# Kernel optimization log

Measured on AMD Instinct MI355X. Metric: run time of the kernel, lower is better.

Reference implementation:

```python
import jax, jax.numpy as jnp
import numpy as np

B, L = 4, 2048
D_MODEL = 64          # d_model = input_size
ED = 128              # d_inner = expand_factor * d_model = hidden_size
N = 32                # d_state
DCONV = 16            # d_conv
NLAYERS = 4
DTRANK = 4            # ceil(d_model/16)
NCLS = 1
EPS = 1e-5


def setup_inputs() -> dict:
    key = jax.random.key(0)
    ks = jax.random.split(key, 10)
    g = lambda k, s, sc: jax.random.normal(k, s, dtype=jnp.float32) * sc
    inp = {}
    inp["x"] = jax.random.normal(ks[0], (B, L, D_MODEL), dtype=jnp.float32)
    inp["in_w"] = g(ks[1], (NLAYERS, 2 * ED, D_MODEL), 0.1)
    inp["in_b"] = jnp.zeros((NLAYERS, 2 * ED), jnp.float32)
    inp["conv_w"] = g(ks[2], (NLAYERS, ED, 1, DCONV), 0.1)  # depthwise kernel (OIH per group)
    inp["conv_b"] = jnp.zeros((NLAYERS, ED), jnp.float32)
    inp["xproj_w"] = g(ks[3], (NLAYERS, DTRANK + 2 * N, ED), 0.1)
    inp["dtproj_w"] = g(ks[4], (NLAYERS, ED, DTRANK), 0.5)
    inp["dtproj_b"] = g(ks[5], (NLAYERS, ED), 0.5)
    # S4D-real init: A[e, n] = n+1
    A = jnp.tile(jnp.arange(1, N + 1, dtype=jnp.float32), (ED, 1))
    inp["A_log"] = jnp.tile(jnp.log(A)[None], (NLAYERS, 1, 1))
    inp["Dp"] = jnp.ones((NLAYERS, ED), jnp.float32)
    inp["outproj_w"] = g(ks[6], (NLAYERS, D_MODEL, ED), 0.1)
    inp["outproj_b"] = jnp.zeros((NLAYERS, D_MODEL), jnp.float32)
    inp["norm_w"] = jnp.ones((NLAYERS, D_MODEL), jnp.float32)
    inp["fc_w"] = g(ks[7], (NCLS, ED), 0.1)
    inp["fc_b"] = jnp.zeros((NCLS,), jnp.float32)
    return inp


def _rmsnorm(x, w):
    return x * jax.lax.rsqrt(jnp.mean(x * x, axis=-1, keepdims=True) + EPS) * w


def _causal_dwconv(x, w, b):
    # x: [B,L,ED], w: [ED,1,DCONV] depthwise, causal left pad
    xt = jnp.swapaxes(x, 1, 2)  # [B,ED,L]
    y = jax.lax.conv_general_dilated(
        xt, w, window_strides=(1,), padding=[(DCONV - 1, 0)],
        dimension_numbers=("NCH", "OIH", "NCH"), feature_group_count=ED)
    return jnp.swapaxes(y, 1, 2) + b


def _mamba_block(h, in_w, in_b, conv_w, conv_b, xproj_w, dtproj_w, dtproj_b,
                 A_log, Dp, outproj_w, outproj_b, last):
    xz = jnp.einsum("bld,ed->ble", h, in_w) + in_b          # [B,L,2ED]
    xin, z = jnp.split(xz, 2, axis=-1)
    xc = jax.nn.silu(_causal_dwconv(xin, conv_w, conv_b))    # [B,L,ED]
    dbc = jnp.einsum("ble,re->blr", xc, xproj_w)             # [B,L,DTRANK+2N]
    delta = dbc[..., :DTRANK]
    Bm = dbc[..., DTRANK:DTRANK + N]                          # [B,L,N]
    Cm = dbc[..., DTRANK + N:]                                # [B,L,N]
    delta = jax.nn.softplus(jnp.einsum("blr,er->ble", delta, dtproj_w) + dtproj_b)
    A = -jnp.exp(A_log)                                       # [ED,N]
    dA = jnp.exp(delta[..., None] * A)                        # [B,L,ED,N]
    dBu = delta[..., None] * Bm[:, :, None, :] * xc[..., None]  # [B,L,ED,N]

    def step(hs, t):
        dA_t, dBu_t, C_t = t                                  # [B,ED,N],[B,ED,N],[B,N]
        hs = dA_t * hs + dBu_t
        y = jnp.einsum("ben,bn->be", hs, C_t)
        return hs, y

    h0 = jnp.zeros((xc.shape[0], ED, N), dtype=xc.dtype)
    _, ys = jax.lax.scan(step, h0, (jnp.swapaxes(dA, 0, 1),
                                    jnp.swapaxes(dBu, 0, 1),
                                    jnp.swapaxes(Cm, 0, 1)))
    y = jnp.swapaxes(ys, 0, 1) + Dp * xc                      # [B,L,ED]
    y = y * jax.nn.silu(z)
    if last:
        return y                                              # classifier taps d_inner features
    return jnp.einsum("ble,de->bld", y, outproj_w) + outproj_b


def reference(x, in_w, in_b, conv_w, conv_b, xproj_w, dtproj_w, dtproj_b,
              A_log, Dp, outproj_w, outproj_b, norm_w, fc_w, fc_b):
    h = x
    for i in range(NLAYERS - 1):
        h = h + _mamba_block(_rmsnorm(h, norm_w[i]), in_w[i], in_b[i], conv_w[i],
                             conv_b[i], xproj_w[i], dtproj_w[i], dtproj_b[i],
                             A_log[i], Dp[i], outproj_w[i], outproj_b[i], False)
    i = NLAYERS - 1
    y = _mamba_block(_rmsnorm(h, norm_w[i]), in_w[i], in_b[i], conv_w[i],
                     conv_b[i], xproj_w[i], dtproj_w[i], dtproj_b[i],
                     A_log[i], Dp[i], outproj_w[i], outproj_b[i], True)
    last_hidden = y[:, -1, :]                                 # [B,ED]
    return last_hidden @ fc_w.T + fc_b                        # [B,NCLS]
```

## Files before the change

### kernel.cpp

```cpp
#include <hip/hip_runtime.h>
#include <math.h>

#define BSZ 4
#define Lseq 2048
#define DM 64
#define ED 128
#define NST 32
#define DCONVK 16
#define NLAYERS 4
#define DTRANK 4
#define EPSV 1e-5f
#define NC 128
#define LC (Lseq / NC)
#define TT 16

__device__ __forceinline__ float sigf(float x) { return 1.0f / (1.0f + __expf(-x)); }
__device__ __forceinline__ float hsum4(float4 a) { return (a.x + a.y) + (a.z + a.w); }

__global__ __launch_bounds__(256) void k_layer_gemm(
    const float* __restrict__ hin, const float* __restrict__ norm_w,
    const float* __restrict__ in_w, const float* __restrict__ in_b,
    float* __restrict__ xin, float* __restrict__ zb)
{
    const int t0 = blockIdx.x * TT;
    const int tid = threadIdx.x;
    const int lane = tid & 63;
    const int wv = tid >> 6;
    __shared__ __align__(16) float hn[TT][DM];

    const float nw = norm_w[lane];
    float hval[4];
    #pragma unroll
    for (int j = 0; j < 4; ++j)
        hval[j] = hin[(size_t)(t0 + wv * 4 + j) * DM + lane];

    #pragma unroll
    for (int j = 0; j < 4; ++j) {
        float ss = hval[j] * hval[j];
        #pragma unroll
        for (int off = 32; off; off >>= 1) ss += __shfl_xor(ss, off, 64);
        const float sc = rsqrtf(ss * (1.0f / DM) + EPSV);
        hn[wv * 4 + j][lane] = hval[j] * sc * nw;
    }
    __syncthreads();

    {
        float4 w4[16];
        const float4* wr = (const float4*)(in_w + tid * DM);
        #pragma unroll
        for (int i = 0; i < 16; ++i) w4[i] = wr[i];
        const float bias = in_b[tid];
        #pragma unroll 2
        for (int tok = 0; tok < TT; ++tok) {
            const float4* hv4 = (const float4*)&hn[tok][0];
            float4 a4 = make_float4(0.f, 0.f, 0.f, 0.f);
            #pragma unroll
            for (int i = 0; i < 16; ++i) {
                float4 hv = hv4[i];
                a4.x = fmaf(hv.x, w4[i].x, a4.x);
                a4.y = fmaf(hv.y, w4[i].y, a4.y);
                a4.z = fmaf(hv.z, w4[i].z, a4.z);
                a4.w = fmaf(hv.w, w4[i].w, a4.w);
            }
            const float r = bias + hsum4(a4);
            if (tid < ED) xin[(size_t)(t0 + tok) * ED + tid] = r;
            else          zb[(size_t)(t0 + tok) * ED + (tid - ED)] = r;
        }
    }
}

__global__ __launch_bounds__(256) void k_conv_scan(
    const float* __restrict__ xin, const float* __restrict__ conv_w,
    const float* __restrict__ conv_b, const float* __restrict__ xproj_w,
    const float* __restrict__ dtproj_w, const float* __restrict__ dtproj_b,
    const float* __restrict__ A_log,
    float* __restrict__ xc_out, float* __restrict__ delta_out,
    float* __restrict__ Bout, float* __restrict__ Cout,
    float* __restrict__ aprod, float* __restrict__ hloc)
{
    const int blk = blockIdx.x;
    const int b   = blk >> 7;
    const int c   = blk & 127;
    const int l0  = c * TT;
    const size_t t0 = (size_t)b * Lseq + l0;
    const int tid = threadIdx.x;
    __shared__ __align__(16) float xs[(TT + DCONVK - 1) * ED];
    __shared__ __align__(16) float xcs[TT][ED];
    __shared__ __align__(16) float Bs[TT][NST];
    __shared__ float dts[TT][DTRANK];
    float (*dl)[ED] = (float (*)[ED])xs;

    {
        const int NV = (TT + DCONVK - 1) * ED / 4;
        for (int idx4 = tid; idx4 < NV; idx4 += 256) {
            const int row = idx4 >> 5;
            const int lrow = l0 - (DCONVK - 1) + row;
            float4 v = make_float4(0.f, 0.f, 0.f, 0.f);
            if (lrow >= 0)
                v = ((const float4*)(xin + ((size_t)b * Lseq + lrow) * ED))[idx4 & 31];
            ((float4*)xs)[idx4] = v;
        }
    }
    __syncthreads();

    const int e = tid & 127, half = tid >> 7;
    {
        float w[DCONVK];
        {
            const float4* cw = (const float4*)(conv_w + e * DCONVK);
            #pragma unroll
            for (int i = 0; i < 4; ++i) {
                float4 cc = cw[i];
                w[i*4+0] = cc.x; w[i*4+1] = cc.y; w[i*4+2] = cc.z; w[i*4+3] = cc.w;
            }
        }
        const float cb = conv_b[e];
        #pragma unroll 2
        for (int j = 0; j < 8; ++j) {
            const int tok = half * 8 + j;
            float acc = cb;
            #pragma unroll
            for (int k = 0; k < DCONVK; ++k)
                acc = fmaf(xs[(tok + k) * ED + e], w[k], acc);
            const float xcv = acc * sigf(acc);
            xcs[tok][e] = xcv;
            xc_out[(t0 + tok) * ED + e] = xcv;
        }
    }
    __syncthreads();

    {
        const int wv = tid >> 6, lane = tid & 63;
        float4 acc[4];
        #pragma unroll
        for (int j = 0; j < 4; ++j) acc[j] = make_float4(0.f, 0.f, 0.f, 0.f);
        #pragma unroll 1
        for (int p = 0; p < 4; ++p) {
            float4 w4[8];
            const float4* wr = (const float4*)(xproj_w + lane * ED + p * 32);
            #pragma unroll
            for (int i = 0; i < 8; ++i) w4[i] = wr[i];
            #pragma unroll
            for (int j = 0; j < 4; ++j) {
                const float4* yv = (const float4*)&xcs[wv * 4 + j][p * 32];
                #pragma unroll
                for (int i = 0; i < 8; ++i) {
                    float4 hv = yv[i];
                    acc[j].x = fmaf(hv.x, w4[i].x, acc[j].x);
                    acc[j].y = fmaf(hv.y, w4[i].y, acc[j].y);
                    acc[j].z = fmaf(hv.z, w4[i].z, acc[j].z);
                    acc[j].w = fmaf(hv.w, w4[i].w, acc[j].w);
                }
            }
        }
        #pragma unroll
        for (int j = 0; j < 4; ++j) {
            const int tok = wv * 4 + j;
            const float v = hsum4(acc[j]);
            if (lane < DTRANK) {
                dts[tok][lane] = v;
            } else if (lane < DTRANK + NST) {
                Bs[tok][lane - DTRANK] = v;
                Bout[(t0 + tok) * NST + (lane - DTRANK)] = v;
            } else {
                Cout[(t0 + tok) * NST + (lane - DTRANK - NST)] = v;
            }
        }
        {
            const int ridx = lane & 3;
            const int ks   = (lane >> 2) & 3;
            const int tsub = lane >> 4;
            const int r4   = 64 + ridx;
            const int tok  = wv * 4 + tsub;
            const float4* wr = (const float4*)(xproj_w + r4 * ED + ks * 32);
            const float4* yv = (const float4*)&xcs[tok][ks * 32];
            float4 a4 = make_float4(0.f, 0.f, 0.f, 0.f);
            #pragma unroll
            for (int i = 0; i < 8; ++i) {
                float4 hv = yv[i]; float4 wv4 = wr[i];
                a4.x = fmaf(hv.x, wv4.x, a4.x);
                a4.y = fmaf(hv.y, wv4.y, a4.y);
                a4.z = fmaf(hv.z, wv4.z, a4.z);
                a4.w = fmaf(hv.w, wv4.w, a4.w);
            }
            float v = hsum4(a4);
            v += __shfl_xor(v, 4, 64);
            v += __shfl_xor(v, 8, 64);
            if (ks == 0) Cout[(t0 + tok) * NST + (r4 - DTRANK - NST)] = v;
        }
    }
    __syncthreads();

    {
        const float4 dwv = *(const float4*)(dtproj_w + e * DTRANK);
        const float bias = dtproj_b[e];
        #pragma unroll 2
        for (int j = 0; j < 8; ++j) {
            const int tok = half * 8 + j;
            float a = bias;
            a = fmaf(dts[tok][0], dwv.x, a);
            a = fmaf(dts[tok][1], dwv.y, a);
            a = fmaf(dts[tok][2], dwv.z, a);
            a = fmaf(dts[tok][3], dwv.w, a);
            const float sp = fmaxf(a, 0.f) + log1pf(__expf(-fabsf(a)));
            dl[tok][e] = sp;
            delta_out[(t0 + tok) * ED + e] = sp;
        }
    }
    __syncthreads();

    {
        float dsum = 0.f;
        #pragma unroll 4
        for (int l = 0; l < TT; ++l) dsum += dl[l][e];

        #pragma unroll 1
        for (int g = 0; g < 2; ++g) {
            const int n0 = half * 16 + g * 8;
            float Aen[8];
            {
                const float4* a4 = (const float4*)(A_log + e * NST + n0);
                const float4 v0 = a4[0], v1 = a4[1];
                Aen[0] = -__expf(v0.x); Aen[1] = -__expf(v0.y);
                Aen[2] = -__expf(v0.z); Aen[3] = -__expf(v0.w);
                Aen[4] = -__expf(v1.x); Aen[5] = -__expf(v1.y);
                Aen[6] = -__expf(v1.z); Aen[7] = -__expf(v1.w);
            }
            float hs[8];
            #pragma unroll
            for (int k = 0; k < 8; ++k) hs[k] = 0.f;
            #pragma unroll 2
            for (int l = 0; l < TT; ++l) {
                const float de   = dl[l][e];
                const float dexc = de * xcs[l][e];
                const float4 B0 = *(const float4*)&Bs[l][n0];
                const float4 B1 = *(const float4*)&Bs[l][n0 + 4];
                float a;
                a = __expf(de * Aen[0]); hs[0] = fmaf(a, hs[0], B0.x * dexc);
                a = __expf(de * Aen[1]); hs[1] = fmaf(a, hs[1], B0.y * dexc);
                a = __expf(de * Aen[2]); hs[2] = fmaf(a, hs[2], B0.z * dexc);
                a = __expf(de * Aen[3]); hs[3] = fmaf(a, hs[3], B0.w * dexc);
                a = __expf(de * Aen[4]); hs[4] = fmaf(a, hs[4], B1.x * dexc);
                a = __expf(de * Aen[5]); hs[5] = fmaf(a, hs[5], B1.y * dexc);
                a = __expf(de * Aen[6]); hs[6] = fmaf(a, hs[6], B1.z * dexc);
                a = __expf(de * Aen[7]); hs[7] = fmaf(a, hs[7], B1.w * dexc);
            }
            const size_t idx = (((size_t)b * NC + c) * ED + e) * NST + n0;
            *(float4*)(hloc + idx)     = make_float4(hs[0], hs[1], hs[2], hs[3]);
            *(float4*)(hloc + idx + 4) = make_float4(hs[4], hs[5], hs[6], hs[7]);
            *(float4*)(aprod + idx) =
                make_float4(__expf(Aen[0] * dsum), __expf(Aen[1] * dsum),
                            __expf(Aen[2] * dsum), __expf(Aen[3] * dsum));
            *(float4*)(aprod + idx + 4) =
                make_float4(__expf(Aen[4] * dsum), __expf(Aen[5] * dsum),
                            __expf(Aen[6] * dsum), __expf(Aen[7] * dsum));
        }
    }
}

__global__ __launch_bounds__(256) void k_scan_combine(
    const float* __restrict__ aprod, float* __restrict__ hloc,
    float* __restrict__ hend)
{
    const int tid = blockIdx.x * 256 + threadIdx.x;
    const int b = tid >> 12;
    const int en = tid & 4095;
    size_t idx = (size_t)b * NC * (ED * NST) + en;
    float h = 0.f;
    #pragma unroll 4
    for (int c = 0; c < NC; ++c) {
        const float a = aprod[idx];
        const float u = hloc[idx];
        hloc[idx] = h;
        h = fmaf(a, h, u);
        idx += ED * NST;
    }
    hend[(size_t)b * (ED * NST) + en] = h;
}

__global__ __launch_bounds__(256) void k_scan_gemm(
    const float* __restrict__ delta, const float* __restrict__ Bv,
    const float* __restrict__ Cv, const float* __restrict__ xc,
    const float* __restrict__ zbin, const float* __restrict__ A_log,
    const float* __restrict__ Dp, const float* __restrict__ hinit,
    const float* __restrict__ ow, const float* __restrict__ ob,
    const float* __restrict__ hin, const float* __restrict__ norm_w,
    const float* __restrict__ in_w, const float* __restrict__ in_b,
    float* __restrict__ hout, float* __restrict__ xin, float* __restrict__ zb)
{
    const int blk = blockIdx.x;
    const int b   = blk >> 7;
    const int c   = blk & 127;
    const int l0  = c * TT;
    const size_t t0 = (size_t)b * Lseq + l0;
    const int tid = threadIdx.x;
    const int e = tid & 127, half = tid >> 7;

    __shared__ __align__(16) float dlS[TT][ED];
    __shared__ __align__(16) float xcS[TT][ED];
    __shared__ __align__(16) float BsS[TT][NST];
    __shared__ __align__(16) float CsS[TT][NST];
    __shared__ __align__(16) float ys[TT][ED];
    __shared__ __align__(16) float pp[2][TT][ED];
    __shared__ __align__(16) float hn[TT][DM];

    {
        const float4* dsrc = (const float4*)(delta + t0 * ED);
        const float4* xsrc = (const float4*)(xc + t0 * ED);
        float4* ddst = (float4*)&dlS[0][0];
        float4* xdst = (float4*)&xcS[0][0];
        #pragma unroll
        for (int i = 0; i < 2; ++i) {
            ddst[tid + i * 256] = dsrc[tid + i * 256];
            xdst[tid + i * 256] = xsrc[tid + i * 256];
        }
        if (tid < 128) {
            ((float4*)&BsS[0][0])[tid] = ((const float4*)(Bv + t0 * NST))[tid];
            ((float4*)&CsS[0][0])[tid] = ((const float4*)(Cv + t0 * NST))[tid];
        }
    }
    __syncthreads();

    #pragma unroll 1
    for (int g = 0; g < 2; ++g) {
        const int n0 = half * 16 + g * 8;
        float Aen[8];
        {
            const float4* a4 = (const float4*)(A_log + e * NST + n0);
            const float4 v0 = a4[0], v1 = a4[1];
            Aen[0] = -__expf(v0.x); Aen[1] = -__expf(v0.y);
            Aen[2] = -__expf(v0.z); Aen[3] = -__expf(v0.w);
            Aen[4] = -__expf(v1.x); Aen[5] = -__expf(v1.y);
            Aen[6] = -__expf(v1.z); Aen[7] = -__expf(v1.w);
        }
        float hs[8];
        {
            const size_t idx = (((size_t)b * NC + c) * ED + e) * NST + n0;
            const float4 h0 = *(const float4*)(hinit + idx);
            const float4 h1 = *(const float4*)(hinit + idx + 4);
            hs[0] = h0.x; hs[1] = h0.y; hs[2] = h0.z; hs[3] = h0.w;
            hs[4] = h1.x; hs[5] = h1.y; hs[6] = h1.z; hs[7] = h1.w;
        }
        #pragma unroll 2
        for (int l = 0; l < TT; ++l) {
            const float de   = dlS[l][e];
            const float dexc = de * xcS[l][e];
            const float4 B0 = *(const float4*)&BsS[l][n0];
            const float4 B1 = *(const float4*)&BsS[l][n0 + 4];
            const float4 C0 = *(const float4*)&CsS[l][n0];
            const float4 C1 = *(const float4*)&CsS[l][n0 + 4];
            float a, p = 0.f;
            a = __expf(de * Aen[0]); hs[0] = fmaf(a, hs[0], B0.x * dexc); p = fmaf(hs[0], C0.x, p);
            a = __expf(de * Aen[1]); hs[1] = fmaf(a, hs[1], B0.y * dexc); p = fmaf(hs[1], C0.y, p);
            a = __expf(de * Aen[2]); hs[2] = fmaf(a, hs[2], B0.z * dexc); p = fmaf(hs[2], C0.z, p);
            a = __expf(de * Aen[3]); hs[3] = fmaf(a, hs[3], B0.w * dexc); p = fmaf(hs[3], C0.w, p);
            a = __expf(de * Aen[4]); hs[4] = fmaf(a, hs[4], B1.x * dexc); p = fmaf(hs[4], C1.x, p);
            a = __expf(de * Aen[5]); hs[5] = fmaf(a, hs[5], B1.y * dexc); p = fmaf(hs[5], C1.y, p);
            a = __expf(de * Aen[6]); hs[6] = fmaf(a, hs[6], B1.z * dexc); p = fmaf(hs[6], C1.z, p);
            a = __expf(de * Aen[7]); hs[7] = fmaf(a, hs[7], B1.w * dexc); p = fmaf(hs[7], C1.w, p);
            if (g == 0) pp[half][l][e] = p;
            else        pp[half][l][e] += p;
        }
    }
    __syncthreads();
    {
        const float dpe = Dp[e];
        #pragma unroll 2
        for (int j = 0; j < 8; ++j) {
            const int tl = half * 8 + j;
            const size_t tok = t0 + tl;
            const float p = pp[0][tl][e] + pp[1][tl][e];
            const float zi = zbin[tok * ED + e];
            ys[tl][e] = (p + dpe * xcS[tl][e]) * (zi * sigf(zi));
        }
    }
    __syncthreads();

    const int lane = tid & 63;
    const int wv = tid >> 6;
    const float nw = norm_w[lane];
    float hval[4];
    {
        float4 acc[4];
        #pragma unroll
        for (int j = 0; j < 4; ++j) acc[j] = make_float4(0.f, 0.f, 0.f, 0.f);
        #pragma unroll 1
        for (int p = 0; p < 4; ++p) {
            float4 w4[8];
            const float4* wr = (const float4*)(ow + lane * ED + p * 32);
            #pragma unroll
            for (int i = 0; i < 8; ++i) w4[i] = wr[i];
            #pragma unroll
            for (int j = 0; j < 4; ++j) {
                const float4* yv = (const float4*)&ys[wv * 4 + j][p * 32];
                #pragma unroll
                for (int i = 0; i < 8; ++i) {
                    float4 hv = yv[i];
                    acc[j].x = fmaf(hv.x, w4[i].x, acc[j].x);
                    acc[j].y = fmaf(hv.y, w4[i].y, acc[j].y);
                    acc[j].z = fmaf(hv.z, w4[i].z, acc[j].z);
                    acc[j].w = fmaf(hv.w, w4[i].w, acc[j].w);
                }
            }
        }
        const float obd = ob[lane];
        #pragma unroll
        for (int j = 0; j < 4; ++j) {
            const size_t tok = t0 + wv * 4 + j;
            hval[j] = hsum4(acc[j]) + obd + hin[tok * DM + lane];
            hout[tok * DM + lane] = hval[j];
        }
    }
    #pragma unroll
    for (int j = 0; j < 4; ++j) {
        float ss = hval[j] * hval[j];
        #pragma unroll
        for (int off = 32; off; off >>= 1) ss += __shfl_xor(ss, off, 64);
        const float sc = rsqrtf(ss * (1.0f / DM) + EPSV);
        hn[wv * 4 + j][lane] = hval[j] * sc * nw;
    }
    __syncthreads();
    {
        float4 w4[16];
        const float4* wr = (const float4*)(in_w + tid * DM);
        #pragma unroll
        for (int i = 0; i < 16; ++i) w4[i] = wr[i];
        const float bias = in_b[tid];
        #pragma unroll 2
        for (int tok = 0; tok < TT; ++tok) {
            const float4* hv4 = (const float4*)&hn[tok][0];
            float4 a4 = make_float4(0.f, 0.f, 0.f, 0.f);
            #pragma unroll
            for (int i = 0; i < 16; ++i) {
                float4 hv = hv4[i];
                a4.x = fmaf(hv.x, w4[i].x, a4.x);
                a4.y = fmaf(hv.y, w4[i].y, a4.y);
                a4.z = fmaf(hv.z, w4[i].z, a4.z);
                a4.w = fmaf(hv.w, w4[i].w, a4.w);
            }
            const float r = bias + hsum4(a4);
            if (tid < ED) xin[(size_t)(t0 + tok) * ED + tid] = r;
            else          zb[(size_t)(t0 + tok) * ED + (tid - ED)] = r;
        }
    }
}

__global__ __launch_bounds__(128) void k_final_last(
    const float* __restrict__ hend, const float* __restrict__ Cv,
    const float* __restrict__ xc, const float* __restrict__ zb,
    const float* __restrict__ Dp, const float* __restrict__ fcw,
    const float* __restrict__ fcb, float* __restrict__ out)
{
    const int b = blockIdx.x;
    const int e = threadIdx.x;
    const size_t tok = (size_t)b * Lseq + (Lseq - 1);
    const float* hp = hend + (size_t)b * (ED * NST) + e * NST;
    const float* cp = Cv + tok * NST;
    float p = 0.f;
    #pragma unroll
    for (int n = 0; n < NST; ++n) p = fmaf(hp[n], cp[n], p);
    const float xce = xc[tok * ED + e];
    const float zi  = zb[tok * ED + e];
    float val = (p + Dp[e] * xce) * (zi * sigf(zi)) * fcw[e];
    __shared__ float sred[2];
    #pragma unroll
    for (int off = 32; off; off >>= 1) val += __shfl_xor(val, off, 64);
    if ((threadIdx.x & 63) == 0) sred[threadIdx.x >> 6] = val;
    __syncthreads();
    if (threadIdx.x == 0) out[b] = sred[0] + sred[1] + fcb[0];
}

extern "C" void kernel_launch(void* const* d_in, const int* in_sizes, int n_in,
                              void* d_out, int out_size, void* d_ws, size_t ws_size,
                              hipStream_t stream)
{
    const float* x         = (const float*)d_in[0];
    const float* in_w      = (const float*)d_in[1];
    const float* in_b      = (const float*)d_in[2];
    const float* conv_w    = (const float*)d_in[3];
    const float* conv_b    = (const float*)d_in[4];
    const float* xproj_w   = (const float*)d_in[5];
    const float* dtproj_w  = (const float*)d_in[6];
    const float* dtproj_b  = (const float*)d_in[7];
    const float* A_log     = (const float*)d_in[8];
    const float* Dp        = (const float*)d_in[9];
    const float* outproj_w = (const float*)d_in[10];
    const float* outproj_b = (const float*)d_in[11];
    const float* norm_w    = (const float*)d_in[12];
    const float* fc_w      = (const float*)d_in[13];
    const float* fc_b      = (const float*)d_in[14];

    const size_t TOK = (size_t)BSZ * Lseq;
    float* ws = (float*)d_ws;
    float* h0    = ws; ws += TOK * DM;
    float* h1    = ws; ws += TOK * DM;
    float* xin   = ws; ws += TOK * ED;
    float* zbuf  = ws; ws += TOK * ED;
    float* xc    = ws; ws += TOK * ED;
    float* dlt   = ws; ws += TOK * ED;
    float* Bv    = ws; ws += TOK * NST;
    float* Cv    = ws; ws += TOK * NST;
    float* aprod = ws; ws += (size_t)BSZ * NC * ED * NST;
    float* hloc  = ws; ws += (size_t)BSZ * NC * ED * NST;
    float* hend  = ws; ws += (size_t)BSZ * ED * NST;

    const float* hres = x;
    float* hbufs[2] = { h0, h1 };

    k_layer_gemm<<<(int)(TOK / TT), 256, 0, stream>>>(
        x, norm_w, in_w, in_b, xin, zbuf);

    for (int i = 0; i < NLAYERS; ++i) {
        const int last = (i == NLAYERS - 1);
        const float* Alog_i = A_log + (size_t)i * ED * NST;
        k_conv_scan<<<(int)(BSZ * NC), 256, 0, stream>>>(
            xin, conv_w + (size_t)i * ED * DCONVK, conv_b + (size_t)i * ED,
            xproj_w + (size_t)i * (DTRANK + 2 * NST) * ED,
            dtproj_w + (size_t)i * ED * DTRANK, dtproj_b + (size_t)i * ED,
            Alog_i, xc, dlt, Bv, Cv, aprod, hloc);
        k_scan_combine<<<(BSZ * ED * NST) / 256, 256, 0, stream>>>(
            aprod, hloc, hend);
        if (!last) {
            float* hout = hbufs[i & 1];
            k_scan_gemm<<<(int)(BSZ * NC), 256, 0, stream>>>(
                dlt, Bv, Cv, xc, zbuf, Alog_i, Dp + (size_t)i * ED, hloc,
                outproj_w + (size_t)i * DM * ED, outproj_b + (size_t)i * DM,
                hres, norm_w + (size_t)(i + 1) * DM,
                in_w + (size_t)(i + 1) * 2 * ED * DM,
                in_b + (size_t)(i + 1) * 2 * ED,
                hout, xin, zbuf);
            hres = hout;
        } else {
            k_final_last<<<BSZ, 128, 0, stream>>>(
                hend, Cv, xc, zbuf, Dp + (size_t)i * ED, fc_w, fc_b, (float*)d_out);
        }
    }
}
```

Baseline: 382.9 us.

## Fuse all Mamba layers into one persistent cooperative kernel with grid syncs

Replaces the sequence of per-layer kernel launches with a single cooperative kernel of 512 blocks that loops over layers and separates phases with grid.sync(). Per-block intermediates (conv output, delta, B, C, residual) stay in shared memory and registers, so the global round-trips for xc, delta, B, C and the residual stream are no longer needed. It also removes about a dozen launch gaps. The cost is grid-wide barriers, and the chunk-combine phase runs on only 64 blocks while the rest wait. If the cooperative launch fails, the code falls back to the old multi-kernel path.

New measurement: 1.106 ms. 189% more time.

```diff
diff --git a/kernel.cpp b/kernel.cpp
--- a/kernel.cpp
+++ b/kernel.cpp
@@ -1,5 +1,8 @@
 #include <hip/hip_runtime.h>
+#include <hip/hip_cooperative_groups.h>
 #include <math.h>
+
+namespace cg = cooperative_groups;
 
 #define BSZ 4
 #define Lseq 2048
@@ -11,11 +14,392 @@
 #define DTRANK 4
 #define EPSV 1e-5f
 #define NC 128
-#define LC (Lseq / NC)
 #define TT 16
 
 __device__ __forceinline__ float sigf(float x) { return 1.0f / (1.0f + __expf(-x)); }
 __device__ __forceinline__ float hsum4(float4 a) { return (a.x + a.y) + (a.z + a.w); }
+
+struct Params {
+    const float *x, *in_w, *in_b, *conv_w, *conv_b, *xproj_w, *dtproj_w, *dtproj_b;
+    const float *A_log, *Dp, *outproj_w, *outproj_b, *norm_w, *fc_w, *fc_b;
+    float *out, *xin, *zbuf, *aprod, *hloc, *hend;
+};
+
+__device__ __forceinline__ void inproj16(
+    const float* in_w_l, const float* in_b_l, const float (*hn)[DM],
+    float* xin, float* zbuf, size_t t0, int tid)
+{
+    float4 w4[16];
+    const float4* wr = (const float4*)(in_w_l + tid * DM);
+    #pragma unroll
+    for (int i = 0; i < 16; ++i) w4[i] = wr[i];
+    const float bias = in_b_l[tid];
+    #pragma unroll 2
+    for (int tok = 0; tok < TT; ++tok) {
+        const float4* hv4 = (const float4*)&hn[tok][0];
+        float4 a4 = make_float4(0.f, 0.f, 0.f, 0.f);
+        #pragma unroll
+        for (int i = 0; i < 16; ++i) {
+            float4 hv = hv4[i];
+            a4.x = fmaf(hv.x, w4[i].x, a4.x);
+            a4.y = fmaf(hv.y, w4[i].y, a4.y);
+            a4.z = fmaf(hv.z, w4[i].z, a4.z);
+            a4.w = fmaf(hv.w, w4[i].w, a4.w);
+        }
+        const float r = bias + hsum4(a4);
+        if (tid < ED) xin[(t0 + tok) * ED + tid] = r;
+        else          zbuf[(t0 + tok) * ED + (tid - ED)] = r;
+    }
+}
+
+__global__ __launch_bounds__(256) void k_mamba_fused(Params P)
+{
+    cg::grid_group grid = cg::this_grid();
+    const int blk = blockIdx.x;
+    const int b   = blk >> 7;
+    const int c   = blk & 127;
+    const int l0  = c * TT;
+    const size_t t0 = (size_t)b * Lseq + l0;
+    const int tid = threadIdx.x;
+    const int e = tid & 127, half = tid >> 7;
+    const int lane = tid & 63, wv = tid >> 6;
+    const int e2 = tid >> 1, nh = tid & 1;
+
+    __shared__ __align__(16) float smem[7168];
+    float (*xcs)[ED] = (float (*)[ED])smem;
+    float (*Bs)[NST] = (float (*)[NST])(smem + 2048);
+    float (*Cs)[NST] = (float (*)[NST])(smem + 2560);
+    float* uni = smem + 3072;
+    float* xs = uni;
+    float (*dts)[DTRANK] = (float (*)[DTRANK])(uni + 3968);
+    float (*dl)[ED] = (float (*)[ED])uni;
+    float (*ys)[ED] = (float (*)[ED])(uni + 2048);
+    float (*hn)[DM] = (float (*)[DM])(smem + 2048);
+    float* sred = uni;
+
+    float hres[4];
+
+    {
+        const float nw = P.norm_w[lane];
+        #pragma unroll
+        for (int j = 0; j < 4; ++j)
+            hres[j] = P.x[(size_t)(t0 + wv * 4 + j) * DM + lane];
+        #pragma unroll
+        for (int j = 0; j < 4; ++j) {
+            float ss = hres[j] * hres[j];
+            #pragma unroll
+            for (int off = 32; off; off >>= 1) ss += __shfl_xor(ss, off, 64);
+            const float sc = rsqrtf(ss * (1.0f / DM) + EPSV);
+            hn[wv * 4 + j][lane] = hres[j] * sc * nw;
+        }
+        __syncthreads();
+        inproj16(P.in_w, P.in_b, hn, P.xin, P.zbuf, t0, tid);
+    }
+    grid.sync();
+
+    #pragma unroll 1
+    for (int i = 0; i < NLAYERS; ++i) {
+        const float* conv_w_i = P.conv_w + (size_t)i * ED * DCONVK;
+        const float* conv_b_i = P.conv_b + (size_t)i * ED;
+        const float* xproj_i  = P.xproj_w + (size_t)i * (DTRANK + 2 * NST) * ED;
+        const float* dtw_i    = P.dtproj_w + (size_t)i * ED * DTRANK;
+        const float* dtb_i    = P.dtproj_b + (size_t)i * ED;
+        const float* Alog_i   = P.A_log + (size_t)i * ED * NST;
+        const float* Dp_i     = P.Dp + (size_t)i * ED;
+
+        {
+            const int NV = (TT + DCONVK - 1) * ED / 4;
+            for (int idx4 = tid; idx4 < NV; idx4 += 256) {
+                const int row = idx4 >> 5;
+                const int lrow = l0 - (DCONVK - 1) + row;
+                float4 v = make_float4(0.f, 0.f, 0.f, 0.f);
+                if (lrow >= 0)
+                    v = ((const float4*)(P.xin + ((size_t)b * Lseq + lrow) * ED))[idx4 & 31];
+                ((float4*)xs)[idx4] = v;
+            }
+        }
+        __syncthreads();
+        {
+            float w[DCONVK];
+            {
+                const float4* cw = (const float4*)(conv_w_i + e * DCONVK);
+                #pragma unroll
+                for (int q = 0; q < 4; ++q) {
+                    float4 cc = cw[q];
+                    w[q*4+0] = cc.x; w[q*4+1] = cc.y; w[q*4+2] = cc.z; w[q*4+3] = cc.w;
+                }
+            }
+            const float cb = conv_b_i[e];
+            #pragma unroll 2
+            for (int j = 0; j < 8; ++j) {
+                const int tok = half * 8 + j;
+                float acc = cb;
+                #pragma unroll
+                for (int k = 0; k < DCONVK; ++k)
+                    acc = fmaf(xs[(tok + k) * ED + e], w[k], acc);
+                const float xcv = acc * sigf(acc);
+                xcs[tok][e] = xcv;
+            }
+        }
+        __syncthreads();
+        {
+            float4 acc[4];
+            #pragma unroll
+            for (int j = 0; j < 4; ++j) acc[j] = make_float4(0.f, 0.f, 0.f, 0.f);
+            #pragma unroll 1
+            for (int p = 0; p < 4; ++p) {
+                float4 w4[8];
+                const float4* wr = (const float4*)(xproj_i + lane * ED + p * 32);
+                #pragma unroll
+                for (int q = 0; q < 8; ++q) w4[q] = wr[q];
+                #pragma unroll
+                for (int j = 0; j < 4; ++j) {
+                    const float4* yv = (const float4*)&xcs[wv * 4 + j][p * 32];
+                    #pragma unroll
+                    for (int q = 0; q < 8; ++q) {
+                        float4 hv = yv[q];
+                        acc[j].x = fmaf(hv.x, w4[q].x, acc[j].x);
+                        acc[j].y = fmaf(hv.y, w4[q].y, acc[j].y);
+                        acc[j].z = fmaf(hv.z, w4[q].z, acc[j].z);
+                        acc[j].w = fmaf(hv.w, w4[q].w, acc[j].w);
+                    }
+                }
+            }
+            #pragma unroll
+            for (int j = 0; j < 4; ++j) {
+                const int tok = wv * 4 + j;
+                const float v = hsum4(acc[j]);
+                if (lane < DTRANK)            dts[tok][lane] = v;
+                else if (lane < DTRANK + NST) Bs[tok][lane - DTRANK] = v;
+                else                          Cs[tok][lane - DTRANK - NST] = v;
+            }
+            {
+                const int ridx = lane & 3;
+                const int ks   = (lane >> 2) & 3;
+                const int tsub = lane >> 4;
+                const int r4   = 64 + ridx;
+                const int tok  = wv * 4 + tsub;
+                const float4* wr = (const float4*)(xproj_i + r4 * ED + ks * 32);
+                const float4* yv = (const float4*)&xcs[tok][ks * 32];
+                float4 a4 = make_float4(0.f, 0.f, 0.f, 0.f);
+                #pragma unroll
+                for (int q = 0; q < 8; ++q) {
+                    float4 hv = yv[q]; float4 wv4 = wr[q];
+                    a4.x = fmaf(hv.x, wv4.x, a4.x);
+                    a4.y = fmaf(hv.y, wv4.y, a4.y);
+                    a4.z = fmaf(hv.z, wv4.z, a4.z);
+                    a4.w = fmaf(hv.w, wv4.w, a4.w);
+                }
+                float v = hsum4(a4);
+                v += __shfl_xor(v, 4, 64);
+                v += __shfl_xor(v, 8, 64);
+                if (ks == 0) Cs[tok][r4 - DTRANK - NST] = v;
+            }
+        }
+        __syncthreads();
+        {
+            const float4 dwv = *(const float4*)(dtw_i + e * DTRANK);
+            const float bias = dtb_i[e];
+            #pragma unroll 2
+            for (int j = 0; j < 8; ++j) {
+                const int tok = half * 8 + j;
+                float a = bias;
+                a = fmaf(dts[tok][0], dwv.x, a);
+                a = fmaf(dts[tok][1], dwv.y, a);
+                a = fmaf(dts[tok][2], dwv.z, a);
+                a = fmaf(dts[tok][3], dwv.w, a);
+                dl[tok][e] = fmaxf(a, 0.f) + log1pf(__expf(-fabsf(a)));
+            }
+        }
+        __syncthreads();
+        {
+            float dsum = 0.f;
+            #pragma unroll 4
+            for (int l = 0; l < TT; ++l) dsum += dl[l][e2];
+            #pragma unroll 1
+            for (int g = 0; g < 2; ++g) {
+                const int n0 = nh * 16 + g * 8;
+                float Aen[8];
+                {
+                    const float4* a4 = (const float4*)(Alog_i + e2 * NST + n0);
+                    const float4 v0 = a4[0], v1 = a4[1];
+                    Aen[0] = -__expf(v0.x); Aen[1] = -__expf(v0.y);
+                    Aen[2] = -__expf(v0.z); Aen[3] = -__expf(v0.w);
+                    Aen[4] = -__expf(v1.x); Aen[5] = -__expf(v1.y);
+                    Aen[6] = -__expf(v1.z); Aen[7] = -__expf(v1.w);
+                }
+                float hs[8];
+                #pragma unroll
+                for (int k = 0; k < 8; ++k) hs[k] = 0.f;
+                #pragma unroll 2
+                for (int l = 0; l < TT; ++l) {
+                    const float de   = dl[l][e2];
+                    const float dexc = de * xcs[l][e2];
+                    const float4 B0 = *(const float4*)&Bs[l][n0];
+                    const float4 B1 = *(const float4*)&Bs[l][n0 + 4];
+                    float a;
+                    a = __expf(de * Aen[0]); hs[0] = fmaf(a, hs[0], B0.x * dexc);
+                    a = __expf(de * Aen[1]); hs[1] = fmaf(a, hs[1], B0.y * dexc);
+                    a = __expf(de * Aen[2]); hs[2] = fmaf(a, hs[2], B0.z * dexc);
+                    a = __expf(de * Aen[3]); hs[3] = fmaf(a, hs[3], B0.w * dexc);
+                    a = __expf(de * Aen[4]); hs[4] = fmaf(a, hs[4], B1.x * dexc);
+                    a = __expf(de * Aen[5]); hs[5] = fmaf(a, hs[5], B1.y * dexc);
+                    a = __expf(de * Aen[6]); hs[6] = fmaf(a, hs[6], B1.z * dexc);
+                    a = __expf(de * Aen[7]); hs[7] = fmaf(a, hs[7], B1.w * dexc);
+                }
+                const size_t idx = (((size_t)b * NC + c) * ED + e2) * NST + n0;
+                *(float4*)(P.hloc + idx)     = make_float4(hs[0], hs[1], hs[2], hs[3]);
+                *(float4*)(P.hloc + idx + 4) = make_float4(hs[4], hs[5], hs[6], hs[7]);
+                *(float4*)(P.aprod + idx) =
+                    make_float4(__expf(Aen[0] * dsum), __expf(Aen[1] * dsum),
+                                __expf(Aen[2] * dsum), __expf(Aen[3] * dsum));
+                *(float4*)(P.aprod + idx + 4) =
+                    make_float4(__expf(Aen[4] * dsum), __expf(Aen[5] * dsum),
+                                __expf(Aen[6] * dsum), __expf(Aen[7] * dsum));
+            }
+        }
+        grid.sync();
+
+        if (blk < (BSZ * ED * NST) / 256) {
+            const int gtid = blk * 256 + tid;
+            const int bb = gtid >> 12;
+            const int en = gtid & 4095;
+            size_t idx = (size_t)bb * NC * (ED * NST) + en;
+            float h = 0.f;
+            #pragma unroll 4
+            for (int cc = 0; cc < NC; ++cc) {
+                const float a = P.aprod[idx];
+                const float u = P.hloc[idx];
+                P.hloc[idx] = h;
+                h = fmaf(a, h, u);
+                idx += ED * NST;
+            }
+            P.hend[(size_t)bb * (ED * NST) + en] = h;
+        }
+        grid.sync();
+
+        if (i < NLAYERS - 1) {
+            #pragma unroll 1
+            for (int g = 0; g < 2; ++g) {
+                const int n0 = nh * 16 + g * 8;
+                float Aen[8];
+                {
+                    const float4* a4 = (const float4*)(Alog_i + e2 * NST + n0);
+                    const float4 v0 = a4[0], v1 = a4[1];
+                    Aen[0] = -__expf(v0.x); Aen[1] = -__expf(v0.y);
+                    Aen[2] = -__expf(v0.z); Aen[3] = -__expf(v0.w);
+                    Aen[4] = -__expf(v1.x); Aen[5] = -__expf(v1.y);
+                    Aen[6] = -__expf(v1.z); Aen[7] = -__expf(v1.w);
+                }
+                float hs[8];
+                {
+                    const size_t idx = (((size_t)b * NC + c) * ED + e2) * NST + n0;
+                    const float4 h0 = *(const float4*)(P.hloc + idx);
+                    const float4 h1 = *(const float4*)(P.hloc + idx + 4);
+                    hs[0] = h0.x; hs[1] = h0.y; hs[2] = h0.z; hs[3] = h0.w;
+                    hs[4] = h1.x; hs[5] = h1.y; hs[6] = h1.z; hs[7] = h1.w;
+                }
+                #pragma unroll 2
+                for (int l = 0; l < TT; ++l) {
+                    const float de   = dl[l][e2];
+                    const float dexc = de * xcs[l][e2];
+                    const float4 B0 = *(const float4*)&Bs[l][n0];
+                    const float4 B1 = *(const float4*)&Bs[l][n0 + 4];
+                    const float4 C0 = *(const float4*)&Cs[l][n0];
+                    const float4 C1 = *(const float4*)&Cs[l][n0 + 4];
+                    float a, p = 0.f;
+                    a = __expf(de * Aen[0]); hs[0] = fmaf(a, hs[0], B0.x * dexc); p = fmaf(hs[0], C0.x, p);
+                    a = __expf(de * Aen[1]); hs[1] = fmaf(a, hs[1], B0.y * dexc); p = fmaf(hs[1], C0.y, p);
+                    a = __expf(de * Aen[2]); hs[2] = fmaf(a, hs[2], B0.z * dexc); p = fmaf(hs[2], C0.z, p);
+                    a = __expf(de * Aen[3]); hs[3] = fmaf(a, hs[3], B0.w * dexc); p = fmaf(hs[3], C0.w, p);
+                    a = __expf(de * Aen[4]); hs[4] = fmaf(a, hs[4], B1.x * dexc); p = fmaf(hs[4], C1.x, p);
+                    a = __expf(de * Aen[5]); hs[5] = fmaf(a, hs[5], B1.y * dexc); p = fmaf(hs[5], C1.y, p);
+                    a = __expf(de * Aen[6]); hs[6] = fmaf(a, hs[6], B1.z * dexc); p = fmaf(hs[6], C1.z, p);
+                    a = __expf(de * Aen[7]); hs[7] = fmaf(a, hs[7], B1.w * dexc); p = fmaf(hs[7], C1.w, p);
+                    const float pt = p + __shfl_xor(p, 1, 64);
+                    if (nh == 0) {
+                        if (g == 0) ys[l][e2] = pt;
+                        else        ys[l][e2] += pt;
+                    }
+                }
+            }
+            __syncthreads();
+            {
+                const float dpe = Dp_i[e];
+                #pragma unroll 2
+                for (int j = 0; j < 8; ++j) {
+                    const int tl = half * 8 + j;
+                    const float zi = P.zbuf[(t0 + tl) * ED + e];
+                    ys[tl][e] = (ys[tl][e] + dpe * xcs[tl][e]) * (zi * sigf(zi));
+                }
+            }
+            __syncthreads();
+            const float* ow = P.outproj_w + (size_t)i * DM * ED;
+            const float nw = P.norm_w[(size_t)(i + 1) * DM + lane];
+            {
+                float4 acc[4];
+                #pragma unroll
+                for (int j = 0; j < 4; ++j) acc[j] = make_float4(0.f, 0.f, 0.f, 0.f);
+                #pragma unroll 1
+                for (int p = 0; p < 4; ++p) {
+                    float4 w4[8];
+                    const float4* wr = (const float4*)(ow + lane * ED + p * 32);
+                    #pragma unroll
+                    for (int q = 0; q < 8; ++q) w4[q] = wr[q];
+                    #pragma unroll
+                    for (int j = 0; j < 4; ++j) {
+                        const float4* yv = (const float4*)&ys[wv * 4 + j][p * 32];
+                        #pragma unroll
+                        for (int q = 0; q < 8; ++q) {
+                            float4 hv = yv[q];
+                            acc[j].x = fmaf(hv.x, w4[q].x, acc[j].x);
+                            acc[j].y = fmaf(hv.y, w4[q].y, acc[j].y);
+                            acc[j].z = fmaf(hv.z, w4[q].z, acc[j].z);
+                            acc[j].w = fmaf(hv.w, w4[q].w, acc[j].w);
+                        }
+                    }
+                }
+                const float obd = P.outproj_b[(size_t)i * DM + lane];
+                #pragma unroll
+                for (int j = 0; j < 4; ++j)
+                    hres[j] = hsum4(acc[j]) + obd + hres[j];
+            }
+            __syncthreads();
+            #pragma unroll
+            for (int j = 0; j < 4; ++j) {
+                float ss = hres[j] * hres[j];
+                #pragma unroll
+                for (int off = 32; off; off >>= 1) ss += __shfl_xor(ss, off, 64);
+                const float sc = rsqrtf(ss * (1.0f / DM) + EPSV);
+                hn[wv * 4 + j][lane] = hres[j] * sc * nw;
+            }
+            __syncthreads();
+            inproj16(P.in_w + (size_t)(i + 1) * 2 * ED * DM,
+                     P.in_b + (size_t)(i + 1) * 2 * ED,
+                     (const float (*)[DM])hn, P.xin, P.zbuf, t0, tid);
+            grid.sync();
+        } else {
+            if (c == NC - 1) {
+                float val = 0.f;
+                if (tid < ED) {
+                    const float* hp = P.hend + (size_t)b * (ED * NST) + tid * NST;
+                    float p = 0.f;
+                    #pragma unroll
+                    for (int n = 0; n < NST; ++n) p = fmaf(hp[n], Cs[TT - 1][n], p);
+                    const float xce = xcs[TT - 1][tid];
+                    const float zi  = P.zbuf[(t0 + TT - 1) * ED + tid];
+                    val = (p + Dp_i[tid] * xce) * (zi * sigf(zi)) * P.fc_w[tid];
+                }
+                #pragma unroll
+                for (int off = 32; off; off >>= 1) val += __shfl_xor(val, off, 64);
+                if (lane == 0) sred[wv] = val;
+                __syncthreads();
+                if (tid == 0)
+                    P.out[b] = sred[0] + sred[1] + sred[2] + sred[3] + P.fc_b[0];
+            }
+        }
+    }
+}
 
 __global__ __launch_bounds__(256) void k_layer_gemm(
     const float* __restrict__ hin, const float* __restrict__ norm_w,
@@ -43,30 +427,7 @@
         hn[wv * 4 + j][lane] = hval[j] * sc * nw;
     }
     __syncthreads();
-
-    {
-        float4 w4[16];
-        const float4* wr = (const float4*)(in_w + tid * DM);
-        #pragma unroll
-        for (int i = 0; i < 16; ++i) w4[i] = wr[i];
-        const float bias = in_b[tid];
-        #pragma unroll 2
-        for (int tok = 0; tok < TT; ++tok) {
-            const float4* hv4 = (const float4*)&hn[tok][0];
-            float4 a4 = make_float4(0.f, 0.f, 0.f, 0.f);
-            #pragma unroll
-            for (int i = 0; i < 16; ++i) {
-                float4 hv = hv4[i];
-                a4.x = fmaf(hv.x, w4[i].x, a4.x);
-                a4.y = fmaf(hv.y, w4[i].y, a4.y);
-                a4.z = fmaf(hv.z, w4[i].z, a4.z);
-                a4.w = fmaf(hv.w, w4[i].w, a4.w);
-            }
-            const float r = bias + hsum4(a4);
-            if (tid < ED) xin[(size_t)(t0 + tok) * ED + tid] = r;
-            else          zb[(size_t)(t0 + tok) * ED + (tid - ED)] = r;
-        }
-    }
+    inproj16(in_w, in_b, (const float (*)[DM])hn, xin, zb, (size_t)t0, tid);
 }
 
 __global__ __launch_bounds__(256) void k_conv_scan(
@@ -389,17 +750,17 @@
             float4 w4[8];
             const float4* wr = (const float4*)(ow + lane * ED + p * 32);
             #pragma unroll
-            for (int i = 0; i < 8; ++i) w4[i] = wr[i];
+            for (int q = 0; q < 8; ++q) w4[q] = wr[q];
             #pragma unroll
             for (int j = 0; j < 4; ++j) {
                 const float4* yv = (const float4*)&ys[wv * 4 + j][p * 32];
                 #pragma unroll
-                for (int i = 0; i < 8; ++i) {
-                    float4 hv = yv[i];
-                    acc[j].x = fmaf(hv.x, w4[i].x, acc[j].x);
-                    acc[j].y = fmaf(hv.y, w4[i].y, acc[j].y);
-                    acc[j].z = fmaf(hv.z, w4[i].z, acc[j].z);
-                    acc[j].w = fmaf(hv.w, w4[i].w, acc[j].w);
+                for (int q = 0; q < 8; ++q) {
+                    float4 hv = yv[q];
+                    acc[j].x = fmaf(hv.x, w4[q].x, acc[j].x);
+                    acc[j].y = fmaf(hv.y, w4[q].y, acc[j].y);
+                    acc[j].z = fmaf(hv.z, w4[q].z, acc[j].z);
+                    acc[j].w = fmaf(hv.w, w4[q].w, acc[j].w);
                 }
             }
         }
@@ -420,29 +781,7 @@
         hn[wv * 4 + j][lane] = hval[j] * sc * nw;
     }
     __syncthreads();
-    {
-        float4 w4[16];
-        const float4* wr = (const float4*)(in_w + tid * DM);
-        #pragma unroll
-        for (int i = 0; i < 16; ++i) w4[i] = wr[i];
-        const float bias = in_b[tid];
-        #pragma unroll 2
-        for (int tok = 0; tok < TT; ++tok) {
-            const float4* hv4 = (const float4*)&hn[tok][0];
-            float4 a4 = make_float4(0.f, 0.f, 0.f, 0.f);
-            #pragma unroll
-            for (int i = 0; i < 16; ++i) {
-                float4 hv = hv4[i];
-                a4.x = fmaf(hv.x, w4[i].x, a4.x);
-                a4.y = fmaf(hv.y, w4[i].y, a4.y);
-                a4.z = fmaf(hv.z, w4[i].z, a4.z);
-                a4.w = fmaf(hv.w, w4[i].w, a4.w);
-            }
-            const float r = bias + hsum4(a4);
-            if (tid < ED) xin[(size_t)(t0 + tok) * ED + tid] = r;
-            else          zb[(size_t)(t0 + tok) * ED + (tid - ED)] = r;
-        }
-    }
+    inproj16(in_w, in_b, (const float (*)[DM])hn, xin, zb, t0, tid);
 }
 
 __global__ __launch_bounds__(128) void k_final_last(
@@ -492,47 +831,60 @@
 
     const size_t TOK = (size_t)BSZ * Lseq;
     float* ws = (float*)d_ws;
+    float* xin   = ws; ws += TOK * ED;
+    float* zbuf  = ws; ws += TOK * ED;
+    float* aprod = ws; ws += (size_t)BSZ * NC * ED * NST;
+    float* hloc  = ws; ws += (size_t)BSZ * NC * ED * NST;
+    float* hend  = ws; ws += (size_t)BSZ * ED * NST;
     float* h0    = ws; ws += TOK * DM;
     float* h1    = ws; ws += TOK * DM;
-    float* xin   = ws; ws += TOK * ED;
-    float* zbuf  = ws; ws += TOK * ED;
     float* xc    = ws; ws += TOK * ED;
     float* dlt   = ws; ws += TOK * ED;
     float* Bv    = ws; ws += TOK * NST;
     float* Cv    = ws; ws += TOK * NST;
-    float* aprod = ws; ws += (size_t)BSZ * NC * ED * NST;
-    float* hloc  = ws; ws += (size_t)BSZ * NC * ED * NST;
-    float* hend  = ws; ws += (size_t)BSZ * ED * NST;
-
-    const float* hres = x;
-    float* hbufs[2] = { h0, h1 };
-
-    k_layer_gemm<<<(int)(TOK / TT), 256, 0, stream>>>(
-        x, norm_w, in_w, in_b, xin, zbuf);
-
-    for (int i = 0; i < NLAYERS; ++i) {
-        const int last = (i == NLAYERS - 1);
-        const float* Alog_i = A_log + (size_t)i * ED * NST;
-        k_conv_scan<<<(int)(BSZ * NC), 256, 0, stream>>>(
-            xin, conv_w + (size_t)i * ED * DCONVK, conv_b + (size_t)i * ED,
-            xproj_w + (size_t)i * (DTRANK + 2 * NST) * ED,
-            dtproj_w + (size_t)i * ED * DTRANK, dtproj_b + (size_t)i * ED,
-            Alog_i, xc, dlt, Bv, Cv, aprod, hloc);
-        k_scan_combine<<<(BSZ * ED * NST) / 256, 256, 0, stream>>>(
-            aprod, hloc, hend);
-        if (!last) {
-            float* hout = hbufs[i & 1];
-            k_scan_gemm<<<(int)(BSZ * NC), 256, 0, stream>>>(
-                dlt, Bv, Cv, xc, zbuf, Alog_i, Dp + (size_t)i * ED, hloc,
-                outproj_w + (size_t)i * DM * ED, outproj_b + (size_t)i * DM,
-                hres, norm_w + (size_t)(i + 1) * DM,
-                in_w + (size_t)(i + 1) * 2 * ED * DM,
-                in_b + (size_t)(i + 1) * 2 * ED,
-                hout, xin, zbuf);
-            hres = hout;
-        } else {
-            k_final_last<<<BSZ, 128, 0, stream>>>(
-                hend, Cv, xc, zbuf, Dp + (size_t)i * ED, fc_w, fc_b, (float*)d_out);
+
+    Params P;
+    P.x = x; P.in_w = in_w; P.in_b = in_b; P.conv_w = conv_w; P.conv_b = conv_b;
+    P.xproj_w = xproj_w; P.dtproj_w = dtproj_w; P.dtproj_b = dtproj_b;
+    P.A_log = A_log; P.Dp = Dp; P.outproj_w = outproj_w; P.outproj_b = outproj_b;
+    P.norm_w = norm_w; P.fc_w = fc_w; P.fc_b = fc_b;
+    P.out = (float*)d_out; P.xin = xin; P.zbuf = zbuf;
+    P.aprod = aprod; P.hloc = hloc; P.hend = hend;
+
+    void* args[] = { (void*)&P };
+    hipError_t err = hipLaunchCooperativeKernel((const void*)k_mamba_fused,
+                                                dim3(BSZ * NC), dim3(256),
+                                                args, 0, stream);
+    if (err != hipSuccess) {
+        (void)hipGetLastError();
+        const float* hres = x;
+        float* hbufs[2] = { h0, h1 };
+        k_layer_gemm<<<(int)(TOK / TT), 256, 0, stream>>>(
+            x, norm_w, in_w, in_b, xin, zbuf);
+        for (int i = 0; i < NLAYERS; ++i) {
+            const int last = (i == NLAYERS - 1);
+            const float* Alog_i = A_log + (size_t)i * ED * NST;
+            k_conv_scan<<<(int)(BSZ * NC), 256, 0, stream>>>(
+                xin, conv_w + (size_t)i * ED * DCONVK, conv_b + (size_t)i * ED,
+                xproj_w + (size_t)i * (DTRANK + 2 * NST) * ED,
+                dtproj_w + (size_t)i * ED * DTRANK, dtproj_b + (size_t)i * ED,
+                Alog_i, xc, dlt, Bv, Cv, aprod, hloc);
+            k_scan_combine<<<(BSZ * ED * NST) / 256, 256, 0, stream>>>(
+                aprod, hloc, hend);
+            if (!last) {
+                float* hout = hbufs[i & 1];
+                k_scan_gemm<<<(int)(BSZ * NC), 256, 0, stream>>>(
+                    dlt, Bv, Cv, xc, zbuf, Alog_i, Dp + (size_t)i * ED, hloc,
+                    outproj_w + (size_t)i * DM * ED, outproj_b + (size_t)i * DM,
+                    hres, norm_w + (size_t)(i + 1) * DM,
+                    in_w + (size_t)(i + 1) * 2 * ED * DM,
+                    in_b + (size_t)(i + 1) * 2 * ED,
+                    hout, xin, zbuf);
+                hres = hout;
+            } else {
+                k_final_last<<<BSZ, 128, 0, stream>>>(
+                    hend, Cv, xc, zbuf, Dp + (size_t)i * ED, fc_w, fc_b, (float*)d_out);
+            }
         }
     }
 }
```
